# Performance work log

Measured on AMD Instinct MI355X. Metric: run time of the kernel, lower is better.

The kernel has to match this reference:

```python
import jax, jax.numpy as jnp
import numpy as np
import math

DIM = 1024
D_IN = 2048      # expand * dim
N = 16           # d_state
NG = 32          # ngroups
DT_RANK = 64     # ceil(dim/16)
D_CONV = 4
B, L = 2, 1024


def setup_inputs() -> dict:
    key = jax.random.key(0)
    ks = jax.random.split(key, 10)
    nrm = lambda k, shp, s: jax.random.normal(k, shp, jnp.float32) * s
    x = jax.random.normal(ks[0], (B, L, DIM), jnp.float32)
    latent = jnp.zeros((B, NG, D_IN, N), jnp.float32)
    W_in = nrm(ks[1], (2 * D_IN, DIM), 0.02)          # in_proj (no bias)
    conv_w = nrm(ks[2], (D_IN, 1, D_CONV), 0.1)        # depthwise conv weight
    conv_b = nrm(ks[3], (D_IN,), 0.02)                 # conv bias
    W_x = nrm(ks[4], (DT_RANK + 2 * N, D_IN), 0.02)    # x_proj (no bias)
    W_dt = nrm(ks[5], (D_IN, DT_RANK), 0.02)           # dt_proj weight
    b_dt = nrm(ks[6], (D_IN,), 0.1)                    # dt_proj bias
    W_out = nrm(ks[7], (DIM, D_IN), 0.02)              # out_proj (no bias)
    A_log = jnp.log(jnp.tile(jnp.arange(1, N + 1, dtype=jnp.float32), (D_IN, 1)))
    D = jnp.ones((D_IN,), jnp.float32)
    W_cattn = nrm(ks[8], (3 * N, N), 0.02)             # c_attn (no bias)
    return dict(x=x, latent=latent, W_in=W_in, conv_w=conv_w, conv_b=conv_b,
                W_x=W_x, W_dt=W_dt, b_dt=b_dt, W_out=W_out, A_log=A_log,
                D=D, W_cattn=W_cattn)


def _scan_op(e1, e2):
    a1, b1 = e1
    a2, b2 = e2
    return a2 * a1, a2 * b1 + b2


def reference(x, latent, W_in, conv_w, conv_b, W_x, W_dt, b_dt, W_out, A_log, D, W_cattn):
    b, l, _ = x.shape
    xr = x @ W_in.T                                  # [b,l,2*d_in]
    u, res = xr[..., :D_IN], xr[..., D_IN:]
    # depthwise causal conv1d (padding d_conv-1 then truncate to l == left-pad)
    uc = jnp.transpose(u, (0, 2, 1))                 # [b,d_in,l]
    uc = jax.lax.conv_general_dilated(
        uc, conv_w, window_strides=(1,), padding=[(D_CONV - 1, 0)],
        feature_group_count=D_IN, dimension_numbers=('NCH', 'OIH', 'NCH'))
    uc = uc + conv_b[None, :, None]
    u = jax.nn.silu(jnp.transpose(uc, (0, 2, 1)))    # [b,l,d_in]

    A = -jnp.exp(A_log)                              # [d_in,n]
    x_dbl = u @ W_x.T                                # [b,l,dt_rank+2n]
    delta = jax.nn.softplus(x_dbl[..., :DT_RANK] @ W_dt.T + b_dt)  # [b,l,d_in]
    Bm = x_dbl[..., DT_RANK:DT_RANK + N]             # [b,l,n]
    Cm = x_dbl[..., DT_RANK + N:]                    # [b,l,n]

    dA = jnp.exp(delta[..., None] * A)               # [b,l,d_in,n]
    dBu = delta[..., None] * Bm[:, :, None, :] * u[..., None]  # [b,l,d_in,n]

    pg = l // NG
    dA = dA.reshape(b, NG, pg, D_IN, N)
    dBu = dBu.reshape(b, NG, pg, D_IN, N)
    Cg = Cm.reshape(b, NG, pg, N)
    dBu = dBu.at[:, :, 0].add(latent)                # inject group latent

    # parallel scan of h_t = dA_t * h_{t-1} + dBu_t within each group
    _, hs = jax.lax.associative_scan(_scan_op, (dA, dBu), axis=2)
    y = jnp.einsum('bgpdn,bgpn->bgpd', hs, Cg).reshape(b, l, D_IN)
    y = y + u * D

    # latent communication: causal attention over group latents (initial latent, per source)
    qkv = latent[:, :-1] @ W_cattn.T                 # [b,ng-1,d_in,3n]
    q, k, v = jnp.split(qkv, 3, axis=-1)
    G = NG - 1
    q = q.reshape(b, G, -1)
    k = k.reshape(b, G, -1)
    v = v.reshape(b, G, -1)
    scale = 1.0 / math.sqrt(D_IN * N)
    scores = (q @ jnp.swapaxes(k, 1, 2)) * scale     # [b,G,G]
    mask = jnp.tril(jnp.ones((G, G), bool))
    scores = jnp.where(mask, scores, -jnp.inf)
    attn = jax.nn.softmax(scores, axis=-1)
    lat = (attn @ v).reshape(b, G, D_IN, N)
    lat_out = jnp.concatenate([jnp.zeros((b, 1, D_IN, N), x.dtype), lat], axis=1)

    out = (y * jax.nn.silu(res)) @ W_out.T           # [b,l,dim]
    return out, lat_out
```

## Files before the change

kernel.cpp:

```cpp
#include <hip/hip_runtime.h>
#include <stdint.h>

typedef uint16_t u16;
typedef u16   u16x4  __attribute__((ext_vector_type(4)));
typedef u16   u16x8  __attribute__((ext_vector_type(8)));
typedef __bf16 bf16x8 __attribute__((ext_vector_type(8)));
typedef float f32x4  __attribute__((ext_vector_type(4)));

__device__ __forceinline__ float b2f(u16 x) {
    union { uint32_t u; float f; } c; c.u = ((uint32_t)x) << 16; return c.f;
}
__device__ __forceinline__ u16 f2b(float f) {
    union { float f; uint32_t u; } c; c.f = f;
    uint32_t r = c.u + 0x7FFFu + ((c.u >> 16) & 1u);
    return (u16)(r >> 16);
}
__device__ __forceinline__ float silu_f(float x) { return x / (1.f + __expf(-x)); }
__device__ __forceinline__ float softplus_f(float x) {
    return fmaxf(x, 0.f) + __logf(1.f + __expf(-fabsf(x)));
}

__device__ __forceinline__ void gload16(const u16* g, u16* l) {
    __builtin_amdgcn_global_load_lds(
        (const __attribute__((address_space(1))) void*)(g),
        (__attribute__((address_space(3))) void*)(l), 16, 0, 0);
}

__device__ __forceinline__ int dtype_flag_block(const u16* __restrict__ xraw) {
    __shared__ int bad;
    if (threadIdx.x == 0) bad = 0;
    __syncthreads();
    float v = b2f(xraw[threadIdx.x]);
    if (!(fabsf(v) < 1000.f)) atomicAdd(&bad, 1);
    __syncthreads();
    return bad;
}

struct CvtArgs {
    const void* s[13];
    u16* d[13];
    int cum[14];
    int total;
};
__global__ __launch_bounds__(256) void cvt_all_k(CvtArgs a, const u16* __restrict__ xraw)
{
    int flag = dtype_flag_block(xraw);
    int u4 = blockIdx.x * 256 + threadIdx.x;
    if (u4 >= a.total) return;
    int seg = 0;
    while (u4 >= a.cum[seg + 1]) seg++;
    int local = u4 - a.cum[seg];
    const void* s = a.s[seg];
    u16x4 o;
    if (s == nullptr) {
        o[0] = o[1] = o[2] = o[3] = 0;
    } else if (flag) {
        f32x4 vv = ((const f32x4*)s)[local];
        for (int e = 0; e < 4; e++) o[e] = f2b(vv[e]);
    } else {
        o = ((const u16x4*)s)[local];
    }
    *(u16x4*)(a.d[seg] + (size_t)local * 4) = o;
}

template<int EPI, int TN>
__device__ __forceinline__ void gemm_core(
    int bx, int by, int bz,
    const u16* __restrict__ A, const u16* __restrict__ B,
    int Kc, int lda, int ldb,
    u16* __restrict__ Cb, float* __restrict__ Cf, int ldc, int ncols,
    size_t zslab)
{
    constexpr int NJ = TN / 32;
    constexpr int BT = TN / 32;
    __shared__ __align__(16) u16 lA[128 * 64];
    __shared__ __align__(16) u16 lB[TN * 64];
    const int tid  = threadIdx.x;
    const int wave = tid >> 6, lane = tid & 63;
    const int quad = lane >> 4, l16 = lane & 15;
    const int wm = wave & 1, wn = wave >> 1;
    const int row0 = by * 128, col0 = bx * TN;
    const int kbeg = bz * Kc;

    f32x4 acc[4][NJ];
    const f32x4 zf = {0.f, 0.f, 0.f, 0.f};
    for (int i = 0; i < 4; i++) for (int j = 0; j < NJ; j++) acc[i][j] = zf;

    const u16* Ap[4]; const u16* Bp[BT];
    int lbaseA[4], lbaseB[BT];
    for (int t = 0; t < 4; t++) {
        int c = t * 256 + tid;
        int r = c >> 3, s = c & 7;
        int q = (s - (r >> 1)) & 7;
        Ap[t] = A + (size_t)(row0 + r) * lda + q * 8 + kbeg;
        lbaseA[t] = (t * 256 + wave * 64) * 8;
    }
    for (int t = 0; t < BT; t++) {
        int c = t * 256 + tid;
        int r = c >> 3, s = c & 7;
        int q = (s - (r >> 1)) & 7;
        Bp[t] = B + (size_t)(col0 + r) * ldb + q * 8 + kbeg;
        lbaseB[t] = (t * 256 + wave * 64) * 8;
    }

    for (int k0 = 0; k0 < Kc; k0 += 64) {
        for (int t = 0; t < 4; t++) gload16(Ap[t] + k0, &lA[lbaseA[t]]);
        for (int t = 0; t < BT; t++) gload16(Bp[t] + k0, &lB[lbaseB[t]]);
        __syncthreads();
        for (int half = 0; half < 2; half++) {
            bf16x8 af[4], bfr[NJ];
            for (int i = 0; i < 4; i++) {
                int r = wm * 64 + i * 16 + l16;
                int s = (half * 4 + quad + (r >> 1)) & 7;
                af[i] = *(const bf16x8*)&lA[r * 64 + s * 8];
            }
            for (int j = 0; j < NJ; j++) {
                int r = wn * (TN / 2) + j * 16 + l16;
                int s = (half * 4 + quad + (r >> 1)) & 7;
                bfr[j] = *(const bf16x8*)&lB[r * 64 + s * 8];
            }
            for (int i = 0; i < 4; i++)
                for (int j = 0; j < NJ; j++)
                    acc[i][j] = __builtin_amdgcn_mfma_f32_16x16x32_bf16(af[i], bfr[j], acc[i][j], 0, 0, 0);
        }
        __syncthreads();
    }

    float* dstf = (EPI == 2) ? (Cf + (size_t)bz * zslab) : Cf;
    for (int i = 0; i < 4; i++) {
        int mb = row0 + wm * 64 + i * 16 + quad * 4;
        for (int j = 0; j < NJ; j++) {
            int n = col0 + wn * (TN / 2) + j * 16 + l16;
            if (n >= ncols) continue;
            if (EPI == 0) {
                for (int v = 0; v < 4; v++)
                    Cb[(size_t)(mb + v) * ldc + n] = f2b(acc[i][j][v]);
            } else {
                for (int v = 0; v < 4; v++)
                    dstf[(size_t)(mb + v) * ldc + n] = acc[i][j][v];
            }
        }
    }
}

template<int EPI, int TN>
__global__ __launch_bounds__(256) void gemm_bt(
    const u16* __restrict__ A, const u16* __restrict__ B,
    int Kc, int lda, int ldb,
    u16* __restrict__ Cb, float* __restrict__ Cf, int ldc, int ncols,
    size_t zslab)
{
    gemm_core<EPI, TN>(blockIdx.x, blockIdx.y, blockIdx.z,
                       A, B, Kc, lda, ldb, Cb, Cf, ldc, ncols, zslab);
}

__global__ __launch_bounds__(256) void redc_k(
    const float* __restrict__ part, u16* __restrict__ dst)
{
    int gid = blockIdx.x * 256 + threadIdx.x;
    int idx = gid * 4;
    f32x4 s = {0.f, 0.f, 0.f, 0.f};
    for (int sl = 0; sl < 16; sl++) {
        f32x4 p = *(const f32x4*)&part[(size_t)sl * 262144 + idx];
        for (int e = 0; e < 4; e++) s[e] += p[e];
    }
    u16x4 o;
    for (int e = 0; e < 4; e++) o[e] = f2b(s[e]);
    *(u16x4*)&dst[idx] = o;
}

__global__ __launch_bounds__(256) void conv_silu_k(
    const u16* __restrict__ xr, const u16* __restrict__ cw,
    const u16* __restrict__ cb, u16* __restrict__ u)
{
    int tid = threadIdx.x;
    int bl  = blockIdx.x;
    int l   = bl & 1023;
    int d0  = tid * 8;
    float acc[8];
    u16x8 bias = *(const u16x8*)&cb[d0];
    for (int j = 0; j < 8; j++) acc[j] = b2f(bias[j]);
    union { u16x8 v[4]; u16 s[32]; } wb;
    for (int t = 0; t < 4; t++) wb.v[t] = *(const u16x8*)&cw[d0 * 4 + t * 8];
    for (int t = 0; t < 4; t++) {
        int ls = l - 3 + t;
        if (ls < 0) continue;
        u16x8 xv = *(const u16x8*)&xr[(size_t)(bl - 3 + t) * 4096 + d0];
        for (int j = 0; j < 8; j++) acc[j] += b2f(xv[j]) * b2f(wb.s[j * 4 + t]);
    }
    u16x8 o;
    for (int j = 0; j < 8; j++) o[j] = f2b(silu_f(acc[j]));
    *(u16x8*)&u[(size_t)bl * 2048 + d0] = o;
}

__global__ __launch_bounds__(256) void scan_qkv_k(
    const u16* __restrict__ u, const u16* __restrict__ xr,
    const u16* __restrict__ xdbl, const u16* __restrict__ Wdt,
    const u16* __restrict__ bdt,
    const u16* __restrict__ latent, const u16* __restrict__ Alog,
    const u16* __restrict__ Dp, u16* __restrict__ yg,
    const u16* __restrict__ Wc, u16* __restrict__ q, u16* __restrict__ k,
    u16* __restrict__ v)
{
    __shared__ __align__(16) u16 lsh[36864];
    int tid = threadIdx.x;
    int bid = blockIdx.x;
    if (bid < 512) {
        u16* lA = lsh;
        u16* lB = lsh + 2048;
        float* dls = (float*)(lsh + 18432);
        float (*Bs)[16] = (float(*)[16])(lsh + 34816);
        float (*Cs)[16] = (float(*)[16])(lsh + 35840);
        const int wave = tid >> 6, lane = tid & 63;
        const int quad = lane >> 4, l16 = lane & 15;
        int dblk = bid & 7, bg = bid >> 3;
        int d = dblk * 256 + tid;

        {
            int r = tid >> 3, s = tid & 7;
            int qg = (s - (r >> 1)) & 7;
            gload16(&xdbl[(size_t)(bg * 32 + r) * 128 + qg * 8], &lA[(wave * 64) * 8]);
        }
        for (int t = 0; t < 8; t++) {
            int c = t * 256 + tid;
            int r = c >> 3, s = c & 7;
            int qg = (s - (r >> 1)) & 7;
            gload16(&Wdt[(size_t)(dblk * 256 + r) * 64 + qg * 8],
                    &lB[(t * 256 + wave * 64) * 8]);
        }
        for (int idx = tid; idx < 512; idx += 256) {
            int p = idx >> 4, n = idx & 15;
            const u16* xp = &xdbl[(size_t)(bg * 32 + p) * 128];
            Bs[p][n] = b2f(xp[64 + n]);
            Cs[p][n] = b2f(xp[80 + n]);
        }
        __syncthreads();

        f32x4 dacc[2][4];
        const f32x4 zf = {0.f, 0.f, 0.f, 0.f};
        for (int i = 0; i < 2; i++) for (int j = 0; j < 4; j++) dacc[i][j] = zf;
        for (int half = 0; half < 2; half++) {
            bf16x8 af[2], bfr[4];
            for (int i = 0; i < 2; i++) {
                int r = i * 16 + l16;
                int s = (half * 4 + quad + (r >> 1)) & 7;
                af[i] = *(const bf16x8*)&lA[r * 64 + s * 8];
            }
            for (int j = 0; j < 4; j++) {
                int r = wave * 64 + j * 16 + l16;
                int s = (half * 4 + quad + (r >> 1)) & 7;
                bfr[j] = *(const bf16x8*)&lB[r * 64 + s * 8];
            }
            for (int i = 0; i < 2; i++)
                for (int j = 0; j < 4; j++)
                    dacc[i][j] = __builtin_amdgcn_mfma_f32_16x16x32_bf16(af[i], bfr[j], dacc[i][j], 0, 0, 0);
        }
        for (int j = 0; j < 4; j++) {
            int n = wave * 64 + j * 16 + l16;
            float bv = b2f(bdt[dblk * 256 + n]);
            for (int i = 0; i < 2; i++) {
                int mb = i * 16 + quad * 4;
                for (int vv = 0; vv < 4; vv++)
                    dls[(mb + vv) * 256 + n] = softplus_f(dacc[i][j][vv] + bv);
            }
        }
        __syncthreads();

        float a[16], h[16];
        {
            u16x8 a0 = *(const u16x8*)&Alog[(size_t)d * 16];
            u16x8 a1 = *(const u16x8*)&Alog[(size_t)d * 16 + 8];
            u16x8 l0 = *(const u16x8*)&latent[((size_t)bg * 2048 + d) * 16];
            u16x8 l1 = *(const u16x8*)&latent[((size_t)bg * 2048 + d) * 16 + 8];
            for (int n = 0; n < 8; n++) {
                a[n] = -__expf(b2f(a0[n])); a[8 + n] = -__expf(b2f(a1[n]));
                h[n] = b2f(l0[n]);          h[8 + n] = b2f(l1[n]);
            }
        }
        float Dd = b2f(Dp[d]);
        for (int p = 0; p < 32; p++) {
            size_t row = (size_t)bg * 32 + p;
            float dlt = dls[p * 256 + tid];
            float uu  = b2f(u[row * 2048 + d]);
            float db  = dlt * uu;
            float y = 0.f;
            if (p == 0) {
                for (int n = 0; n < 16; n++) { h[n] += db * Bs[0][n]; y += h[n] * Cs[0][n]; }
            } else {
                for (int n = 0; n < 16; n++) {
                    float w = __expf(dlt * a[n]);
                    h[n] = w * h[n] + db * Bs[p][n];
                    y += h[n] * Cs[p][n];
                }
            }
            float rs = b2f(xr[row * 4096 + 2048 + d]);
            yg[row * 2048 + d] = f2b((y + uu * Dd) * silu_f(rs));
        }
    } else {
        float (*Ws)[16] = (float(*)[16])lsh;
        for (int i = tid; i < 768; i += 256) Ws[i >> 4][i & 15] = b2f(Wc[i]);
        __syncthreads();
        int gid = (bid - 512) * 256 + tid;
        int d = gid & 2047;
        int bi = gid >> 11;
        int b = bi / 31, i = bi - b * 31;
        const u16* lp = &latent[(((size_t)b * 32 + i) * 2048 + d) * 16];
        float lv[16];
        {
            u16x8 l0 = *(const u16x8*)lp, l1 = *(const u16x8*)(lp + 8);
            for (int m = 0; m < 8; m++) { lv[m] = b2f(l0[m]); lv[8 + m] = b2f(l1[m]); }
        }
        u16* outs[3] = {q, k, v};
        for (int pl = 0; pl < 3; pl++) {
            u16x8 o0, o1;
            for (int n = 0; n < 16; n++) {
                float s = 0.f;
                for (int m = 0; m < 16; m++) s += lv[m] * Ws[pl * 16 + n][m];
                if (n < 8) o0[n] = f2b(s); else o1[n - 8] = f2b(s);
            }
            u16* op = outs[pl] + (size_t)bi * 32768 + d * 16;
            *(u16x8*)op = o0; *(u16x8*)(op + 8) = o1;
        }
    }
}

__global__ __launch_bounds__(256) void gemm_scores_k(
    const u16* __restrict__ yg, const u16* __restrict__ Wout, float* __restrict__ out_part,
    const u16* __restrict__ q, const u16* __restrict__ kk, float* __restrict__ sc)
{
    int bid = blockIdx.x;
    if (bid < 512) {
        int bx = bid & 15, by = (bid >> 4) & 15, bz = bid >> 8;
        gemm_core<2, 64>(bx, by, bz, yg, Wout, 1024, 2048, 2048,
                         nullptr, out_part, 1024, 1024, (size_t)2048 * 1024);
        return;
    }
    int idx = bid - 512;
    int b = idx / 961, r = idx - b * 961;
    int i = r / 31, j = r - i * 31;
    if (j > i) return;
    const u16* qp = q + ((size_t)b * 31 + i) * 32768;
    const u16* kp = kk + ((size_t)b * 31 + j) * 32768;
    float s = 0.f;
    for (int t = threadIdx.x * 8; t < 32768; t += 2048) {
        u16x8 a = *(const u16x8*)&qp[t];
        u16x8 c = *(const u16x8*)&kp[t];
        for (int e = 0; e < 8; e++) s += b2f(a[e]) * b2f(c[e]);
    }
    for (int off = 32; off; off >>= 1) s += __shfl_xor(s, off);
    __shared__ float red[4];
    if ((threadIdx.x & 63) == 0) red[threadIdx.x >> 6] = s;
    __syncthreads();
    if (threadIdx.x == 0)
        sc[idx] = (red[0] + red[1] + red[2] + red[3]) * 5.5242717e-3f;
}

__global__ __launch_bounds__(256) void attv_redout_k(
    const float* __restrict__ sc, const u16* __restrict__ v,
    const float* __restrict__ part, void* __restrict__ dout,
    const u16* __restrict__ xraw)
{
    int flag = dtype_flag_block(xraw);
    int bid = blockIdx.x;
    if (bid < 1024) {
        int chunk = bid & 15, bi = bid >> 4;
        int b = bi >> 5, i = (bi & 31) - 1;
        __shared__ float as[32];
        if (i >= 0 && threadIdx.x < 64) {
            float x = (threadIdx.x <= i) ? sc[(size_t)b * 961 + i * 31 + threadIdx.x] : -3.4e38f;
            float mx = x;
            for (int off = 32; off; off >>= 1) mx = fmaxf(mx, __shfl_xor(mx, off));
            float e = (threadIdx.x <= i) ? __expf(x - mx) : 0.f;
            float sm = e;
            for (int off = 32; off; off >>= 1) sm += __shfl_xor(sm, off);
            if (threadIdx.x < 32) as[threadIdx.x] = e / sm;
        }
        __syncthreads();
        int dn = chunk * 2048 + threadIdx.x * 8;
        float acc[8] = {0, 0, 0, 0, 0, 0, 0, 0};
        if (i >= 0) {
            for (int j = 0; j <= i; j++) {
                u16x8 vv = *(const u16x8*)&v[((size_t)b * 31 + j) * 32768 + dn];
                float aj = as[j];
                for (int e = 0; e < 8; e++) acc[e] += aj * b2f(vv[e]);
            }
            for (int e = 0; e < 8; e++) if (!(fabsf(acc[e]) < 1e30f)) acc[e] = 0.f;
        }
        size_t ofs = 2097152 + ((size_t)b * 32 + (i + 1)) * 32768 + dn;
        if (flag) {
            f32x4 o0, o1;
            for (int e = 0; e < 4; e++) { o0[e] = acc[e]; o1[e] = acc[4 + e]; }
            *(f32x4*)((float*)dout + ofs) = o0;
            *(f32x4*)((float*)dout + ofs + 4) = o1;
        } else {
            u16x8 o;
            for (int e = 0; e < 8; e++) o[e] = f2b(acc[e]);
            *(u16x8*)((u16*)dout + ofs) = o;
        }
    } else {
        int gid = (bid - 1024) * 256 + threadIdx.x;
        int m = gid >> 8;
        int j = (gid & 255) * 4;
        f32x4 s = {0.f, 0.f, 0.f, 0.f};
        for (int ks = 0; ks < 2; ks++) {
            f32x4 p = *(const f32x4*)&part[((size_t)ks * 2048 + m) * 1024 + j];
            for (int e = 0; e < 4; e++) s[e] += p[e];
        }
        for (int e = 0; e < 4; e++) if (!(fabsf(s[e]) < 1e30f)) s[e] = 0.f;
        if (flag) {
            ((f32x4*)dout)[(size_t)m * 256 + (j >> 2)] = s;
        } else {
            u16x4 o;
            for (int e = 0; e < 4; e++) o[e] = f2b(s[e]);
            ((u16x4*)dout)[(size_t)m * 256 + (j >> 2)] = o;
        }
    }
}

extern "C" void kernel_launch(void* const* d_in, const int* in_sizes, int n_in,
                              void* d_out, int out_size, void* d_ws, size_t ws_size,
                              hipStream_t stream)
{
    char* ws = (char*)d_ws;
    const u16* xraw = (const u16*)d_in[0];
    u16* cx    = (u16*)(ws + 0);
    u16* clat  = (u16*)(ws + 4194304);
    u16* cWin  = (u16*)(ws + 8388608);
    u16* ccw   = (u16*)(ws + 16777216);
    u16* ccb   = (u16*)(ws + 16793600);
    u16* wxp   = (u16*)(ws + 16797696);
    u16* cWdt  = (u16*)(ws + 17321984);
    u16* cbdt  = (u16*)(ws + 17584128);
    u16* cWout = (u16*)(ws + 17588224);
    u16* cAlog = (u16*)(ws + 21782528);
    u16* cD    = (u16*)(ws + 21848064);
    u16* cWc   = (u16*)(ws + 21852160);
    float* xdbl_part = (float*)(ws + 21853760);
    u16*   xdbl      = (u16*)(ws + 38630976);
    float* sc        = (float*)(ws + 39155264);
    u16*   u         = (u16*)(ws + 39163008);
    u16*   xr        = (u16*)(ws + 47551616);
    u16*   yg        = (u16*)(ws + 64328832);
    u16*   qb        = (u16*)(ws + 72717440);
    u16*   kb        = qb + 2031616;
    u16*   vb        = kb + 2031616;
    float* out_part  = (float*)(ws + 84907136);

    CvtArgs ca;
    const void* srcs[13] = { d_in[0], d_in[1], d_in[2], d_in[3], d_in[4],
                             d_in[5], nullptr, d_in[6], d_in[7], d_in[8],
                             d_in[9], d_in[10], d_in[11] };
    u16* dsts[13] = { cx, clat, cWin, ccw, ccb,
                      wxp, wxp + 196608, cWdt, cbdt, cWout,
                      cAlog, cD, cWc };
    int ns[13] = { 2097152, 2097152, 4194304, 8192, 2048,
                   196608, 65536, 131072, 2048, 2097152,
                   32768, 2048, 768 };
    int cum = 0;
    for (int i = 0; i < 13; i++) {
        ca.s[i] = srcs[i]; ca.d[i] = dsts[i];
        ca.cum[i] = cum; cum += ns[i] / 4;
    }
    ca.cum[13] = cum; ca.total = cum;
    cvt_all_k<<<(cum + 255) / 256, 256, 0, stream>>>(ca, xraw);

    gemm_bt<0, 64><<<dim3(64, 16, 1), 256, 0, stream>>>(cx, cWin, 1024, 1024, 1024,
                                                        xr, nullptr, 4096, 4096, 0);
    conv_silu_k<<<2048, 256, 0, stream>>>(xr, ccw, ccb, u);
    gemm_bt<2, 64><<<dim3(2, 16, 16), 256, 0, stream>>>(u, wxp, 128, 2048, 2048,
                                                        nullptr, xdbl_part, 128, 128,
                                                        262144);
    redc_k<<<256, 256, 0, stream>>>(xdbl_part, xdbl);
    scan_qkv_k<<<1008, 256, 0, stream>>>(u, xr, xdbl, cWdt, cbdt, clat, cAlog, cD, yg,
                                         cWc, qb, kb, vb);
    gemm_scores_k<<<2434, 256, 0, stream>>>(yg, cWout, out_part, qb, kb, sc);
    attv_redout_k<<<3072, 256, 0, stream>>>(sc, vb, out_part, d_out, xraw);
}
```

Baseline: 226.2 us.

## Split scan state across lane pairs and compute delta with scalar FMAs

The scan kernel now splits each channel's 16-state recurrence across two lanes (8 states each) and combines the outputs with a cross-half shuffle. This doubles the scan blocks from 512 to 1024 and shrinks shared memory from about 72KB to 8KB, which should raise occupancy. The MFMA delta projection is replaced by per-thread dot products using register-held W_dt rows. The kernel also switches to exp2f with A pre-scaled by log2(e) and prefetches the next u/res values. In exchange, half the lanes idle on the store, and the delta dot products are redundant scalar work.

```diff
diff --git a/kernel.cpp b/kernel.cpp
--- a/kernel.cpp
+++ b/kernel.cpp
@@ -202,105 +202,105 @@
     const u16* __restrict__ Wc, u16* __restrict__ q, u16* __restrict__ k,
     u16* __restrict__ v)
 {
-    __shared__ __align__(16) u16 lsh[36864];
+    __shared__ __align__(16) u16 lsh[4096];
     int tid = threadIdx.x;
     int bid = blockIdx.x;
-    if (bid < 512) {
-        u16* lA = lsh;
-        u16* lB = lsh + 2048;
-        float* dls = (float*)(lsh + 18432);
-        float (*Bs)[16] = (float(*)[16])(lsh + 34816);
-        float (*Cs)[16] = (float(*)[16])(lsh + 35840);
+    if (bid < 1024) {
+        u16* lxb = lsh;
+        float (*Bs)[16] = (float(*)[16])(lsh + 2048);
+        float (*Cs)[16] = (float(*)[16])(lsh + 3072);
         const int wave = tid >> 6, lane = tid & 63;
-        const int quad = lane >> 4, l16 = lane & 15;
-        int dblk = bid & 7, bg = bid >> 3;
-        int d = dblk * 256 + tid;
+        const int nh = lane >> 5;
+        int dblk = bid & 15, bg = bid >> 4;
+        const int d = dblk * 128 + wave * 32 + (lane & 31);
+        const int rowb = bg * 32;
 
         {
-            int r = tid >> 3, s = tid & 7;
-            int qg = (s - (r >> 1)) & 7;
-            gload16(&xdbl[(size_t)(bg * 32 + r) * 128 + qg * 8], &lA[(wave * 64) * 8]);
-        }
-        for (int t = 0; t < 8; t++) {
-            int c = t * 256 + tid;
-            int r = c >> 3, s = c & 7;
-            int qg = (s - (r >> 1)) & 7;
-            gload16(&Wdt[(size_t)(dblk * 256 + r) * 64 + qg * 8],
-                    &lB[(t * 256 + wave * 64) * 8]);
+            int p = tid >> 3, t = tid & 7;
+            *(u16x8*)&lxb[p * 64 + t * 8] =
+                *(const u16x8*)&xdbl[(size_t)(rowb + p) * 128 + t * 8];
         }
         for (int idx = tid; idx < 512; idx += 256) {
             int p = idx >> 4, n = idx & 15;
-            const u16* xp = &xdbl[(size_t)(bg * 32 + p) * 128];
+            const u16* xp = &xdbl[(size_t)(rowb + p) * 128];
             Bs[p][n] = b2f(xp[64 + n]);
             Cs[p][n] = b2f(xp[80 + n]);
         }
         __syncthreads();
 
-        f32x4 dacc[2][4];
-        const f32x4 zf = {0.f, 0.f, 0.f, 0.f};
-        for (int i = 0; i < 2; i++) for (int j = 0; j < 4; j++) dacc[i][j] = zf;
-        for (int half = 0; half < 2; half++) {
-            bf16x8 af[2], bfr[4];
-            for (int i = 0; i < 2; i++) {
-                int r = i * 16 + l16;
-                int s = (half * 4 + quad + (r >> 1)) & 7;
-                af[i] = *(const bf16x8*)&lA[r * 64 + s * 8];
-            }
-            for (int j = 0; j < 4; j++) {
-                int r = wave * 64 + j * 16 + l16;
-                int s = (half * 4 + quad + (r >> 1)) & 7;
-                bfr[j] = *(const bf16x8*)&lB[r * 64 + s * 8];
-            }
-            for (int i = 0; i < 2; i++)
-                for (int j = 0; j < 4; j++)
-                    dacc[i][j] = __builtin_amdgcn_mfma_f32_16x16x32_bf16(af[i], bfr[j], dacc[i][j], 0, 0, 0);
-        }
-        for (int j = 0; j < 4; j++) {
-            int n = wave * 64 + j * 16 + l16;
-            float bv = b2f(bdt[dblk * 256 + n]);
-            for (int i = 0; i < 2; i++) {
-                int mb = i * 16 + quad * 4;
-                for (int vv = 0; vv < 4; vv++)
-                    dls[(mb + vv) * 256 + n] = softplus_f(dacc[i][j][vv] + bv);
-            }
-        }
-        __syncthreads();
-
-        float a[16], h[16];
+        float wdtf[32];
         {
-            u16x8 a0 = *(const u16x8*)&Alog[(size_t)d * 16];
-            u16x8 a1 = *(const u16x8*)&Alog[(size_t)d * 16 + 8];
-            u16x8 l0 = *(const u16x8*)&latent[((size_t)bg * 2048 + d) * 16];
-            u16x8 l1 = *(const u16x8*)&latent[((size_t)bg * 2048 + d) * 16 + 8];
+            const u16* wp = &Wdt[(size_t)d * 64 + nh * 32];
+            u16x8 w0 = *(const u16x8*)wp;
+            u16x8 w1 = *(const u16x8*)(wp + 8);
+            u16x8 w2 = *(const u16x8*)(wp + 16);
+            u16x8 w3 = *(const u16x8*)(wp + 24);
+            for (int e = 0; e < 8; e++) {
+                wdtf[e]      = b2f(w0[e]); wdtf[8 + e]  = b2f(w1[e]);
+                wdtf[16 + e] = b2f(w2[e]); wdtf[24 + e] = b2f(w3[e]);
+            }
+        }
+        float bv = b2f(bdt[d]);
+        float dl[32];
+        #pragma unroll
+        for (int p = 0; p < 32; p++) {
+            float s = 0.f;
+            #pragma unroll
+            for (int t = 0; t < 4; t++) {
+                u16x8 xv = *(const u16x8*)&lxb[p * 64 + nh * 32 + t * 8];
+                for (int e = 0; e < 8; e++) s += b2f(xv[e]) * wdtf[t * 8 + e];
+            }
+            s += __shfl_xor(s, 32);
+            dl[p] = softplus_f(s + bv);
+        }
+
+        const float LOG2E = 1.4426950408889634f;
+        float a_[8], h_[8];
+        {
+            u16x8 av = *(const u16x8*)&Alog[(size_t)d * 16 + nh * 8];
+            u16x8 lv = *(const u16x8*)&latent[((size_t)bg * 2048 + d) * 16 + nh * 8];
             for (int n = 0; n < 8; n++) {
-                a[n] = -__expf(b2f(a0[n])); a[8 + n] = -__expf(b2f(a1[n]));
-                h[n] = b2f(l0[n]);          h[8 + n] = b2f(l1[n]);
+                a_[n] = -__expf(b2f(av[n])) * LOG2E;
+                h_[n] = b2f(lv[n]);
             }
         }
         float Dd = b2f(Dp[d]);
+
+        u16 u_nx = u[(size_t)rowb * 2048 + d];
+        u16 r_nx = xr[(size_t)rowb * 4096 + 2048 + d];
+        #pragma unroll
         for (int p = 0; p < 32; p++) {
-            size_t row = (size_t)bg * 32 + p;
-            float dlt = dls[p * 256 + tid];
-            float uu  = b2f(u[row * 2048 + d]);
+            float uu = b2f(u_nx), rsv = b2f(r_nx);
+            if (p < 31) {
+                u_nx = u[(size_t)(rowb + p + 1) * 2048 + d];
+                r_nx = xr[(size_t)(rowb + p + 1) * 4096 + 2048 + d];
+            }
+            float dlt = dl[p];
             float db  = dlt * uu;
-            float y = 0.f;
+            float y8 = 0.f;
             if (p == 0) {
-                for (int n = 0; n < 16; n++) { h[n] += db * Bs[0][n]; y += h[n] * Cs[0][n]; }
+                #pragma unroll
+                for (int n = 0; n < 8; n++) {
+                    h_[n] += db * Bs[0][nh * 8 + n];
+                    y8 += h_[n] * Cs[0][nh * 8 + n];
+                }
             } else {
-                for (int n = 0; n < 16; n++) {
-                    float w = __expf(dlt * a[n]);
-                    h[n] = w * h[n] + db * Bs[p][n];
-                    y += h[n] * Cs[p][n];
+                #pragma unroll
+                for (int n = 0; n < 8; n++) {
+                    float w = exp2f(dlt * a_[n]);
+                    h_[n] = w * h_[n] + db * Bs[p][nh * 8 + n];
+                    y8 += h_[n] * Cs[p][nh * 8 + n];
                 }
             }
-            float rs = b2f(xr[row * 4096 + 2048 + d]);
-            yg[row * 2048 + d] = f2b((y + uu * Dd) * silu_f(rs));
+            float y = y8 + __shfl_xor(y8, 32);
+            if (nh == 0)
+                yg[(size_t)(rowb + p) * 2048 + d] = f2b((y + uu * Dd) * silu_f(rsv));
         }
     } else {
         float (*Ws)[16] = (float(*)[16])lsh;
         for (int i = tid; i < 768; i += 256) Ws[i >> 4][i & 15] = b2f(Wc[i]);
         __syncthreads();
-        int gid = (bid - 512) * 256 + tid;
+        int gid = (bid - 1024) * 256 + tid;
         int d = gid & 2047;
         int bi = gid >> 11;
         int b = bi / 31, i = bi - b * 31;
@@ -471,7 +471,7 @@
                                                         nullptr, xdbl_part, 128, 128,
                                                         262144);
     redc_k<<<256, 256, 0, stream>>>(xdbl_part, xdbl);
-    scan_qkv_k<<<1008, 256, 0, stream>>>(u, xr, xdbl, cWdt, cbdt, clat, cAlog, cD, yg,
+    scan_qkv_k<<<1520, 256, 0, stream>>>(u, xr, xdbl, cWdt, cbdt, clat, cAlog, cD, yg,
                                          cWc, qb, kb, vb);
     gemm_scores_k<<<2434, 256, 0, stream>>>(yg, cWout, out_part, qb, kb, sc);
     attv_redout_k<<<3072, 256, 0, stream>>>(sc, vb, out_part, d_out, xraw);
```

After: 233.0 us. 3.0% more time.
